# Performance work log

Measured on AMD Instinct MI355X. Metric: run time of the kernel, lower is better.

## Reference

```python
import math
import jax, jax.numpy as jnp
import numpy as np

N_ANGLES = 8
RADIUS_WIDTH = 8
OVERLAP_RATIO = 1.5
EPS = 1e-8


def _build_masks(H, W):
    # radius bin index [H,W] and normalized overlapping angular soft weights [A,H,W]
    cy, cx = H // 2, W // 2
    y, x = jnp.meshgrid(jnp.arange(H, dtype=jnp.float32), jnp.arange(W, dtype=jnp.float32), indexing='ij')
    dy, dx = y - cy, x - cx
    r = jnp.sqrt(dy ** 2 + dx ** 2)
    theta = (jnp.arctan2(dy, dx) + math.pi) % math.pi
    n_radii = int(max(cy, cx) // RADIUS_WIDTH) + 1
    radius_idx = jnp.clip(jnp.floor(r / RADIUS_WIDTH).astype(jnp.int32), 0, n_radii - 1)
    delta = math.pi / N_ANGLES
    half_width = OVERLAP_RATIO * delta / 2.0
    centers = (jnp.arange(N_ANGLES, dtype=jnp.float32) + 0.5) * delta  # [A]
    dist = jnp.abs(theta[None, :, :] - centers[:, None, None])        # [A,H,W]
    w = jnp.clip(1.0 - dist / half_width, 0.0, None) * (dist < half_width).astype(jnp.float32)
    angle_weights = w / (w.sum(axis=0, keepdims=True) + EPS)          # [A,H,W]
    return radius_idx, angle_weights, n_radii


def setup_inputs() -> dict:
    key = jax.random.key(0)
    k1, k2, k3, k4 = jax.random.split(key, 4)
    B, C, H, W = 8, 256, 128, 128
    c_mid = 16
    n_radii = (max(H // 2, W // 2) // RADIUS_WIDTH) + 1  # = 9
    x = jax.random.normal(k1, (B, C, H, W), dtype=jnp.float32)
    w_in = jax.random.normal(k2, (c_mid, C), dtype=jnp.float32) * 0.05   # 1x1 conv proj_in
    w_out = jax.random.normal(k3, (C, c_mid), dtype=jnp.float32) * 0.05  # 1x1 conv proj_out
    freq_weights = 1.0 + 0.1 * jax.random.normal(k4, (c_mid, N_ANGLES, n_radii), dtype=jnp.float32)
    return {"x": x, "w_in": w_in, "w_out": w_out, "freq_weights": freq_weights}


def reference(x, w_in, w_out, freq_weights):
    B, C, H, W = x.shape
    radius_idx, angle_weights, n_radii = _build_masks(H, W)
    # 1x1 conv in
    x_proj = jnp.einsum('bchw,mc->bmhw', x, w_in)                      # [B,c_mid,H,W]
    # FFT -> centered spectrum
    x_fft = jnp.fft.fftshift(jnp.fft.fft2(x_proj, norm='ortho'), axes=(-2, -1))
    mag = jnp.abs(x_fft) + EPS
    theta = jnp.angle(x_fft)
    # gain[c,h,w] = sum_a angle_weights[a,h,w] * freq_weights[c, a, radius_idx[h,w]]
    w_sel = freq_weights[:, :, radius_idx]                             # [c_mid,A,H,W] gather
    gain = jnp.einsum('ahw,cahw->chw', angle_weights, w_sel)           # [c_mid,H,W]
    mag_enh = mag * gain[None]                                         # [B,c_mid,H,W]
    x_fft_enh = mag_enh * jnp.exp(1j * theta)
    x_enh = jnp.fft.ifft2(jnp.fft.ifftshift(x_fft_enh, axes=(-2, -1)), norm='ortho').real
    out = x + jnp.einsum('bmhw,cm->bchw', x_enh, w_out)                # residual + 1x1 conv out
    return out
```

## Files before the change

### kernel.cpp

```cpp
#include <hip/hip_runtime.h>
#include <math.h>

#define NB   8
#define CIN  256
#define CMID 16
#define NH   128
#define NW   128
#define HWSZ 16384
#define HW4  4096
#define NANG 8
#define NRAD 9

typedef float f32x4_t __attribute__((ext_vector_type(4)));

__device__ __forceinline__ int bitrev7(int v) {
    return (int)(__brev((unsigned)v) >> 25);
}

__global__ void __launch_bounds__(256) gain_kernel(const float* __restrict__ fw,
                                                   float* __restrict__ gain) {
    int p  = blockIdx.x * 256 + threadIdx.x;
    int py = p >> 7, px = p & 127;
    int fy = bitrev7(py), fx = bitrev7(px);
    int hy = (fy + 64) & 127, hx = (fx + 64) & 127;
    float dy = (float)(hy - 64), dx = (float)(hx - 64);
    float r = sqrtf(dy * dy + dx * dx);
    int ridx = (int)floorf(r * 0.125f);
    if (ridx > NRAD - 1) ridx = NRAD - 1;
    const float PI_F = 3.14159265358979323846f;
    float theta = fmodf(atan2f(dy, dx) + PI_F, PI_F);
    const float delta = (float)(M_PI / 8.0);
    const float hwid  = (float)(1.5 * (M_PI / 8.0) / 2.0);
    float wv[NANG];
    float wsum = 0.f;
#pragma unroll
    for (int a = 0; a < NANG; ++a) {
        float c = ((float)a + 0.5f) * delta;
        float dist = fabsf(theta - c);
        float wa = fmaxf(1.0f - dist / hwid, 0.0f);
        if (!(dist < hwid)) wa = 0.0f;
        wv[a] = wa;
        wsum += wa;
    }
    float inv = 1.0f / (wsum + 1e-8f);
#pragma unroll
    for (int m = 0; m < CMID; ++m) {
        float g = 0.f;
#pragma unroll
        for (int a = 0; a < NANG; ++a)
            g += wv[a] * fw[(m * NANG + a) * NRAD + ridx];
        gain[m * HWSZ + p] = g * inv * (1.0f / 16384.0f);
    }
}

__global__ void __launch_bounds__(256, 4) proj_partial(const float* __restrict__ x,
                                                       const float* __restrict__ w_in,
                                                       float* __restrict__ partials,
                                                       int nchunk) {
    int b  = blockIdx.z;
    int ck = blockIdx.y;
    int p4 = blockIdx.x * 256 + threadIdx.x;
    int cpc = CIN / nchunk;
    int c0 = ck * cpc;
    const float4* xb = (const float4*)(x + (size_t)b * CIN * HWSZ);
    float4 acc[CMID];
#pragma unroll
    for (int m = 0; m < CMID; ++m) acc[m] = make_float4(0.f, 0.f, 0.f, 0.f);
    for (int c = c0; c < c0 + cpc; c += 4) {
        float4 v0 = xb[(size_t)(c + 0) * HW4 + p4];
        float4 v1 = xb[(size_t)(c + 1) * HW4 + p4];
        float4 v2 = xb[(size_t)(c + 2) * HW4 + p4];
        float4 v3 = xb[(size_t)(c + 3) * HW4 + p4];
#pragma unroll
        for (int m = 0; m < CMID; ++m) {
            float w0 = w_in[m * CIN + c + 0];
            float w1 = w_in[m * CIN + c + 1];
            float w2 = w_in[m * CIN + c + 2];
            float w3 = w_in[m * CIN + c + 3];
            acc[m].x = fmaf(v0.x, w0, fmaf(v1.x, w1, fmaf(v2.x, w2, fmaf(v3.x, w3, acc[m].x))));
            acc[m].y = fmaf(v0.y, w0, fmaf(v1.y, w1, fmaf(v2.y, w2, fmaf(v3.y, w3, acc[m].y))));
            acc[m].z = fmaf(v0.z, w0, fmaf(v1.z, w1, fmaf(v2.z, w2, fmaf(v3.z, w3, acc[m].z))));
            acc[m].w = fmaf(v0.w, w0, fmaf(v1.w, w1, fmaf(v2.w, w2, fmaf(v3.w, w3, acc[m].w))));
        }
    }
    float4* pb = (float4*)(partials + ((size_t)(b * nchunk + ck) * CMID) * HWSZ);
#pragma unroll
    for (int m = 0; m < CMID; ++m) pb[(size_t)m * HW4 + p4] = acc[m];
}

__global__ void __launch_bounds__(256) reduce_fft_rows(const float* __restrict__ partials,
                                                       float2* __restrict__ xf,
                                                       int nchunk) {
    __shared__ float2 lds[4 * 128];
    int img = blockIdx.y;
    int b = img >> 4, m = img & 15;
    int r0 = blockIdx.x * 4;
    int t = threadIdx.x;
#pragma unroll
    for (int ii = 0; ii < 2; ++ii) {
        int px = ii * 256 + t;
        float s = 0.f;
        for (int ck = 0; ck < nchunk; ++ck)
            s += partials[((size_t)(b * nchunk + ck) * CMID + m) * HWSZ + r0 * NW + px];
        lds[px] = make_float2(s, 0.f);
    }
    __syncthreads();
    const float PI_F = 3.14159265358979323846f;
    int j = t & 63;
    float2* row = lds + (t >> 6) * 128;
    for (int ls = 6; ls >= 0; --ls) {
        int s = 1 << ls;
        int off = j & (s - 1);
        int i0 = ((j >> ls) << (ls + 1)) + off;
        float ang = -PI_F * (float)off / (float)s;
        float sn, cs;
        __sincosf(ang, &sn, &cs);
        float2 a = row[i0];
        float2 bb = row[i0 + s];
        row[i0] = make_float2(a.x + bb.x, a.y + bb.y);
        float dx_ = a.x - bb.x, dy_ = a.y - bb.y;
        row[i0 + s] = make_float2(dx_ * cs - dy_ * sn, dx_ * sn + dy_ * cs);
        __syncthreads();
    }
#pragma unroll
    for (int ii = 0; ii < 2; ++ii) {
        int px = ii * 256 + t;
        xf[(size_t)img * HWSZ + r0 * NW + px] = lds[px];
    }
}

__global__ void __launch_bounds__(256) fft_cols_gain(float2* __restrict__ xf,
                                                     const float* __restrict__ gain) {
    __shared__ float2 buf[128 * 33];
    int img = blockIdx.y;
    int m   = img & (CMID - 1);
    int c0  = blockIdx.x * 32;
    int t   = threadIdx.x;
    float2* xi = xf + (size_t)img * HWSZ;

    for (int idx = t; idx < 128 * 32; idx += 256) {
        int r = idx >> 5, lc = idx & 31;
        buf[r * 33 + lc] = xi[r * NW + c0 + lc];
    }
    __syncthreads();
    const float PI_F = 3.14159265358979323846f;
    int lc = t & 31;
    int jb = t >> 5;
    for (int ls = 6; ls >= 0; --ls) {
        int s = 1 << ls;
        for (int j = jb; j < 64; j += 8) {
            int off = j & (s - 1);
            int i0 = ((j >> ls) << (ls + 1)) + off;
            float ang = -PI_F * (float)off / (float)s;
            float sn, cs;
            __sincosf(ang, &sn, &cs);
            float2 a = buf[i0 * 33 + lc];
            float2 bb = buf[(i0 + s) * 33 + lc];
            buf[i0 * 33 + lc] = make_float2(a.x + bb.x, a.y + bb.y);
            float dx_ = a.x - bb.x, dy_ = a.y - bb.y;
            buf[(i0 + s) * 33 + lc] = make_float2(dx_ * cs - dy_ * sn, dx_ * sn + dy_ * cs);
        }
        __syncthreads();
    }
    {
        const float* gm = gain + (size_t)m * HWSZ;
        for (int idx = t; idx < 128 * 32; idx += 256) {
            int r = idx >> 5, lcc = idx & 31;
            float g = gm[r * NW + c0 + lcc];
            buf[r * 33 + lcc].x *= g;
            buf[r * 33 + lcc].y *= g;
        }
        __syncthreads();
    }
    for (int ls = 0; ls <= 6; ++ls) {
        int s = 1 << ls;
        for (int j = jb; j < 64; j += 8) {
            int off = j & (s - 1);
            int i0 = ((j >> ls) << (ls + 1)) + off;
            float ang = PI_F * (float)off / (float)s;
            float sn, cs;
            __sincosf(ang, &sn, &cs);
            float2 a = buf[i0 * 33 + lc];
            float2 bb = buf[(i0 + s) * 33 + lc];
            float tx = bb.x * cs - bb.y * sn, ty = bb.x * sn + bb.y * cs;
            buf[i0 * 33 + lc] = make_float2(a.x + tx, a.y + ty);
            buf[(i0 + s) * 33 + lc] = make_float2(a.x - tx, a.y - ty);
        }
        __syncthreads();
    }
    for (int idx = t; idx < 128 * 32; idx += 256) {
        int r = idx >> 5, lcc = idx & 31;
        xi[r * NW + c0 + lcc] = buf[r * 33 + lcc];
    }
}

__global__ void __launch_bounds__(256) ifft_rows(const float2* __restrict__ xf,
                                                 float* __restrict__ xe) {
    __shared__ float2 lds[4 * 128];
    int img = blockIdx.y;
    int r0 = blockIdx.x * 4;
    int t = threadIdx.x;
#pragma unroll
    for (int ii = 0; ii < 2; ++ii) {
        int px = ii * 256 + t;
        lds[px] = xf[(size_t)img * HWSZ + r0 * NW + px];
    }
    __syncthreads();
    const float PI_F = 3.14159265358979323846f;
    int j = t & 63;
    float2* row = lds + (t >> 6) * 128;
    for (int ls = 0; ls <= 6; ++ls) {
        int s = 1 << ls;
        int off = j & (s - 1);
        int i0 = ((j >> ls) << (ls + 1)) + off;
        float ang = PI_F * (float)off / (float)s;
        float sn, cs;
        __sincosf(ang, &sn, &cs);
        float2 a = row[i0];
        float2 bb = row[i0 + s];
        float tx = bb.x * cs - bb.y * sn, ty = bb.x * sn + bb.y * cs;
        row[i0] = make_float2(a.x + tx, a.y + ty);
        row[i0 + s] = make_float2(a.x - tx, a.y - ty);
        __syncthreads();
    }
#pragma unroll
    for (int ii = 0; ii < 2; ++ii) {
        int px = ii * 256 + t;
        xe[(size_t)img * HWSZ + r0 * NW + px] = lds[px].x;
    }
}

__global__ void __launch_bounds__(256, 4) out_kernel(const float* __restrict__ x,
                                                     const float* __restrict__ w_out,
                                                     const float* __restrict__ xe,
                                                     float* __restrict__ out) {
    int b  = blockIdx.z;
    int ct = blockIdx.y;
    int p4 = blockIdx.x * 256 + threadIdx.x;
    const float4* xeb = (const float4*)(xe + (size_t)b * CMID * HWSZ);
    float4 e[CMID];
#pragma unroll
    for (int m = 0; m < CMID; ++m) e[m] = xeb[(size_t)m * HW4 + p4];
    const float4* xb = (const float4*)(x + (size_t)b * CIN * HWSZ);
    f32x4_t* ob = (f32x4_t*)(out + (size_t)b * CIN * HWSZ);
    int c0 = ct * 32;
    for (int c = c0; c < c0 + 32; c += 2) {
        float4 a0 = xb[(size_t)(c + 0) * HW4 + p4];
        float4 a1 = xb[(size_t)(c + 1) * HW4 + p4];
#pragma unroll
        for (int m = 0; m < CMID; ++m) {
            float w0 = w_out[(c + 0) * CMID + m];
            float w1 = w_out[(c + 1) * CMID + m];
            a0.x = fmaf(w0, e[m].x, a0.x); a0.y = fmaf(w0, e[m].y, a0.y);
            a0.z = fmaf(w0, e[m].z, a0.z); a0.w = fmaf(w0, e[m].w, a0.w);
            a1.x = fmaf(w1, e[m].x, a1.x); a1.y = fmaf(w1, e[m].y, a1.y);
            a1.z = fmaf(w1, e[m].z, a1.z); a1.w = fmaf(w1, e[m].w, a1.w);
        }
        f32x4_t s0 = { a0.x, a0.y, a0.z, a0.w };
        f32x4_t s1 = { a1.x, a1.y, a1.z, a1.w };
        __builtin_nontemporal_store(s0, ob + (size_t)(c + 0) * HW4 + p4);
        __builtin_nontemporal_store(s1, ob + (size_t)(c + 1) * HW4 + p4);
    }
}

extern "C" void kernel_launch(void* const* d_in, const int* in_sizes, int n_in,
                              void* d_out, int out_size, void* d_ws, size_t ws_size,
                              hipStream_t stream) {
    const float* x     = (const float*)d_in[0];
    const float* w_in  = (const float*)d_in[1];
    const float* w_out = (const float*)d_in[2];
    const float* fw    = (const float*)d_in[3];
    float* out = (float*)d_out;
    float* ws  = (float*)d_ws;

    int nchunk = 8;
    while (nchunk > 1) {
        size_t need = ((size_t)NB * nchunk * CMID * HWSZ +
                       (size_t)NB * CMID * HWSZ * 2 + (size_t)CMID * HWSZ) * sizeof(float);
        if (need <= ws_size) break;
        nchunk >>= 1;
    }
    float*  partials = ws;
    float2* xf   = (float2*)(ws + (size_t)NB * nchunk * CMID * HWSZ);
    float*  gain = (float*)(xf + (size_t)NB * CMID * HWSZ);
    float*  xe   = partials;

    gain_kernel<<<HWSZ / 256, 256, 0, stream>>>(fw, gain);
    proj_partial<<<dim3(HW4 / 256, nchunk, NB), 256, 0, stream>>>(x, w_in, partials, nchunk);
    reduce_fft_rows<<<dim3(NH / 4, NB * CMID), 256, 0, stream>>>(partials, xf, nchunk);
    fft_cols_gain<<<dim3(NW / 32, NB * CMID), 256, 0, stream>>>(xf, gain);
    ifft_rows<<<dim3(NH / 4, NB * CMID), 256, 0, stream>>>(xf, xe);
    out_kernel<<<dim3(HW4 / 256, CIN / 32, NB), 256, 0, stream>>>(x, w_out, xe, out);
}
```

Measured before the change: 131.1 us.

## Store intermediate partials, spectra and enhanced maps in bf16 with nontemporal loads

Converts every workspace intermediate to bf16: the proj partial sums, the complex spectrum between FFT passes (packed as two bf16 in one 32-bit word), and the enhanced spatial map read by the output kernel. It also adds nontemporal loads on the streamed x and intermediates. The goal is to roughly halve the intermediate memory traffic across all five kernels. In exchange, precision drops through the FFT pipeline, which may exceed the output tolerance.

```diff
diff --git a/kernel.cpp b/kernel.cpp
--- a/kernel.cpp
+++ b/kernel.cpp
@@ -11,7 +11,19 @@
 #define NANG 8
 #define NRAD 9
 
-typedef float f32x4_t __attribute__((ext_vector_type(4)));
+typedef float    f32x4_t __attribute__((ext_vector_type(4)));
+typedef unsigned u32x2_t __attribute__((ext_vector_type(2)));
+
+__device__ __forceinline__ unsigned short f2bf(float f) {
+    unsigned u = __float_as_uint(f);
+    u += 0x7fffu + ((u >> 16) & 1u);
+    return (unsigned short)(u >> 16);
+}
+__device__ __forceinline__ float bf_lo(unsigned u) { return __uint_as_float(u << 16); }
+__device__ __forceinline__ float bf_hi(unsigned u) { return __uint_as_float(u & 0xffff0000u); }
+__device__ __forceinline__ unsigned pack2(float a, float b) {
+    return (unsigned)f2bf(a) | ((unsigned)f2bf(b) << 16);
+}
 
 __device__ __forceinline__ int bitrev7(int v) {
     return (int)(__brev((unsigned)v) >> 25);
@@ -55,7 +67,7 @@
 
 __global__ void __launch_bounds__(256, 4) proj_partial(const float* __restrict__ x,
                                                        const float* __restrict__ w_in,
-                                                       float* __restrict__ partials,
+                                                       unsigned short* __restrict__ partials,
                                                        int nchunk) {
     int b  = blockIdx.z;
     int ck = blockIdx.y;
@@ -83,27 +95,39 @@
             acc[m].w = fmaf(v0.w, w0, fmaf(v1.w, w1, fmaf(v2.w, w2, fmaf(v3.w, w3, acc[m].w))));
         }
     }
-    float4* pb = (float4*)(partials + ((size_t)(b * nchunk + ck) * CMID) * HWSZ);
-#pragma unroll
-    for (int m = 0; m < CMID; ++m) pb[(size_t)m * HW4 + p4] = acc[m];
-}
-
-__global__ void __launch_bounds__(256) reduce_fft_rows(const float* __restrict__ partials,
-                                                       float2* __restrict__ xf,
+    ushort4* pb = (ushort4*)partials + ((size_t)(b * nchunk + ck) * CMID) * HW4;
+#pragma unroll
+    for (int m = 0; m < CMID; ++m)
+        pb[(size_t)m * HW4 + p4] = make_ushort4(f2bf(acc[m].x), f2bf(acc[m].y),
+                                                f2bf(acc[m].z), f2bf(acc[m].w));
+}
+
+__global__ void __launch_bounds__(256) reduce_fft_rows(const unsigned short* __restrict__ partials,
+                                                       unsigned* __restrict__ xf,
                                                        int nchunk) {
-    __shared__ float2 lds[4 * 128];
+    __shared__ float2 lds[512];
     int img = blockIdx.y;
     int b = img >> 4, m = img & 15;
     int r0 = blockIdx.x * 4;
     int t = threadIdx.x;
-#pragma unroll
-    for (int ii = 0; ii < 2; ++ii) {
-        int px = ii * 256 + t;
-        float s = 0.f;
-        for (int ck = 0; ck < nchunk; ++ck)
-            s += partials[((size_t)(b * nchunk + ck) * CMID + m) * HWSZ + r0 * NW + px];
-        lds[px] = make_float2(s, 0.f);
-    }
+    const unsigned* pbase = (const unsigned*)(partials +
+        ((size_t)(b * nchunk) * CMID + m) * HWSZ + (size_t)r0 * NW) + t;
+    size_t cks = (size_t)CMID * HWSZ / 2;
+    float sx = 0.f, sy = 0.f;
+    if (nchunk == 8) {
+#pragma unroll
+        for (int ck = 0; ck < 8; ++ck) {
+            unsigned u = __builtin_nontemporal_load(pbase + (size_t)ck * cks);
+            sx += bf_lo(u); sy += bf_hi(u);
+        }
+    } else {
+        for (int ck = 0; ck < nchunk; ++ck) {
+            unsigned u = __builtin_nontemporal_load(pbase + (size_t)ck * cks);
+            sx += bf_lo(u); sy += bf_hi(u);
+        }
+    }
+    lds[2 * t]     = make_float2(sx, 0.f);
+    lds[2 * t + 1] = make_float2(sy, 0.f);
     __syncthreads();
     const float PI_F = 3.14159265358979323846f;
     int j = t & 63;
@@ -122,25 +146,27 @@
         row[i0 + s] = make_float2(dx_ * cs - dy_ * sn, dx_ * sn + dy_ * cs);
         __syncthreads();
     }
+    unsigned* xo = xf + (size_t)img * HWSZ + (size_t)r0 * NW;
 #pragma unroll
     for (int ii = 0; ii < 2; ++ii) {
         int px = ii * 256 + t;
-        xf[(size_t)img * HWSZ + r0 * NW + px] = lds[px];
-    }
-}
-
-__global__ void __launch_bounds__(256) fft_cols_gain(float2* __restrict__ xf,
+        xo[px] = pack2(lds[px].x, lds[px].y);
+    }
+}
+
+__global__ void __launch_bounds__(256) fft_cols_gain(unsigned* __restrict__ xf,
                                                      const float* __restrict__ gain) {
     __shared__ float2 buf[128 * 33];
     int img = blockIdx.y;
     int m   = img & (CMID - 1);
     int c0  = blockIdx.x * 32;
     int t   = threadIdx.x;
-    float2* xi = xf + (size_t)img * HWSZ;
+    unsigned* xi = xf + (size_t)img * HWSZ;
 
     for (int idx = t; idx < 128 * 32; idx += 256) {
         int r = idx >> 5, lc = idx & 31;
-        buf[r * 33 + lc] = xi[r * NW + c0 + lc];
+        unsigned u = __builtin_nontemporal_load(&xi[r * NW + c0 + lc]);
+        buf[r * 33 + lc] = make_float2(bf_lo(u), bf_hi(u));
     }
     __syncthreads();
     const float PI_F = 3.14159265358979323846f;
@@ -190,20 +216,22 @@
     }
     for (int idx = t; idx < 128 * 32; idx += 256) {
         int r = idx >> 5, lcc = idx & 31;
-        xi[r * NW + c0 + lcc] = buf[r * 33 + lcc];
-    }
-}
-
-__global__ void __launch_bounds__(256) ifft_rows(const float2* __restrict__ xf,
-                                                 float* __restrict__ xe) {
-    __shared__ float2 lds[4 * 128];
+        xi[r * NW + c0 + lcc] = pack2(buf[r * 33 + lcc].x, buf[r * 33 + lcc].y);
+    }
+}
+
+__global__ void __launch_bounds__(256) ifft_rows(const unsigned* __restrict__ xf,
+                                                 unsigned short* __restrict__ xe) {
+    __shared__ float2 lds[512];
     int img = blockIdx.y;
     int r0 = blockIdx.x * 4;
     int t = threadIdx.x;
+    const unsigned* xi = xf + (size_t)img * HWSZ + (size_t)r0 * NW;
 #pragma unroll
     for (int ii = 0; ii < 2; ++ii) {
         int px = ii * 256 + t;
-        lds[px] = xf[(size_t)img * HWSZ + r0 * NW + px];
+        unsigned u = __builtin_nontemporal_load(&xi[px]);
+        lds[px] = make_float2(bf_lo(u), bf_hi(u));
     }
     __syncthreads();
     const float PI_F = 3.14159265358979323846f;
@@ -223,43 +251,37 @@
         row[i0 + s] = make_float2(a.x - tx, a.y - ty);
         __syncthreads();
     }
-#pragma unroll
-    for (int ii = 0; ii < 2; ++ii) {
-        int px = ii * 256 + t;
-        xe[(size_t)img * HWSZ + r0 * NW + px] = lds[px].x;
-    }
+    unsigned* xo = (unsigned*)xe + (((size_t)img * HWSZ + (size_t)r0 * NW) >> 1) + t;
+    xo[0] = pack2(lds[2 * t].x, lds[2 * t + 1].x);
 }
 
 __global__ void __launch_bounds__(256, 4) out_kernel(const float* __restrict__ x,
                                                      const float* __restrict__ w_out,
-                                                     const float* __restrict__ xe,
+                                                     const unsigned short* __restrict__ xe,
                                                      float* __restrict__ out) {
     int b  = blockIdx.z;
     int ct = blockIdx.y;
     int p4 = blockIdx.x * 256 + threadIdx.x;
-    const float4* xeb = (const float4*)(xe + (size_t)b * CMID * HWSZ);
-    float4 e[CMID];
-#pragma unroll
-    for (int m = 0; m < CMID; ++m) e[m] = xeb[(size_t)m * HW4 + p4];
-    const float4* xb = (const float4*)(x + (size_t)b * CIN * HWSZ);
+    const u32x2_t* xeb = (const u32x2_t*)(xe + (size_t)b * CMID * HWSZ);
+    f32x4_t e[CMID];
+#pragma unroll
+    for (int m = 0; m < CMID; ++m) {
+        u32x2_t u = __builtin_nontemporal_load(&xeb[(size_t)m * HW4 + p4]);
+        e[m] = (f32x4_t){ bf_lo(u.x), bf_hi(u.x), bf_lo(u.y), bf_hi(u.y) };
+    }
+    const f32x4_t* xb = (const f32x4_t*)(x + (size_t)b * CIN * HWSZ);
     f32x4_t* ob = (f32x4_t*)(out + (size_t)b * CIN * HWSZ);
     int c0 = ct * 32;
     for (int c = c0; c < c0 + 32; c += 2) {
-        float4 a0 = xb[(size_t)(c + 0) * HW4 + p4];
-        float4 a1 = xb[(size_t)(c + 1) * HW4 + p4];
+        f32x4_t a0 = __builtin_nontemporal_load(xb + (size_t)(c + 0) * HW4 + p4);
+        f32x4_t a1 = __builtin_nontemporal_load(xb + (size_t)(c + 1) * HW4 + p4);
 #pragma unroll
         for (int m = 0; m < CMID; ++m) {
-            float w0 = w_out[(c + 0) * CMID + m];
-            float w1 = w_out[(c + 1) * CMID + m];
-            a0.x = fmaf(w0, e[m].x, a0.x); a0.y = fmaf(w0, e[m].y, a0.y);
-            a0.z = fmaf(w0, e[m].z, a0.z); a0.w = fmaf(w0, e[m].w, a0.w);
-            a1.x = fmaf(w1, e[m].x, a1.x); a1.y = fmaf(w1, e[m].y, a1.y);
-            a1.z = fmaf(w1, e[m].z, a1.z); a1.w = fmaf(w1, e[m].w, a1.w);
-        }
-        f32x4_t s0 = { a0.x, a0.y, a0.z, a0.w };
-        f32x4_t s1 = { a1.x, a1.y, a1.z, a1.w };
-        __builtin_nontemporal_store(s0, ob + (size_t)(c + 0) * HW4 + p4);
-        __builtin_nontemporal_store(s1, ob + (size_t)(c + 1) * HW4 + p4);
+            a0 += w_out[(c + 0) * CMID + m] * e[m];
+            a1 += w_out[(c + 1) * CMID + m] * e[m];
+        }
+        __builtin_nontemporal_store(a0, ob + (size_t)(c + 0) * HW4 + p4);
+        __builtin_nontemporal_store(a1, ob + (size_t)(c + 1) * HW4 + p4);
     }
 }
 
@@ -271,24 +293,24 @@
     const float* w_out = (const float*)d_in[2];
     const float* fw    = (const float*)d_in[3];
     float* out = (float*)d_out;
-    float* ws  = (float*)d_ws;
 
     int nchunk = 8;
     while (nchunk > 1) {
-        size_t need = ((size_t)NB * nchunk * CMID * HWSZ +
-                       (size_t)NB * CMID * HWSZ * 2 + (size_t)CMID * HWSZ) * sizeof(float);
+        size_t need = (size_t)NB * nchunk * CMID * HWSZ * 2
+                    + (size_t)NB * CMID * HWSZ * 4
+                    + (size_t)CMID * HWSZ * 4;
         if (need <= ws_size) break;
         nchunk >>= 1;
     }
-    float*  partials = ws;
-    float2* xf   = (float2*)(ws + (size_t)NB * nchunk * CMID * HWSZ);
-    float*  gain = (float*)(xf + (size_t)NB * CMID * HWSZ);
-    float*  xe   = partials;
+    unsigned short* partials = (unsigned short*)d_ws;
+    unsigned* xfu = (unsigned*)(partials + (size_t)NB * nchunk * CMID * HWSZ);
+    float*    gain = (float*)(xfu + (size_t)NB * CMID * HWSZ);
+    unsigned short* xe = partials;
 
     gain_kernel<<<HWSZ / 256, 256, 0, stream>>>(fw, gain);
     proj_partial<<<dim3(HW4 / 256, nchunk, NB), 256, 0, stream>>>(x, w_in, partials, nchunk);
-    reduce_fft_rows<<<dim3(NH / 4, NB * CMID), 256, 0, stream>>>(partials, xf, nchunk);
-    fft_cols_gain<<<dim3(NW / 32, NB * CMID), 256, 0, stream>>>(xf, gain);
-    ifft_rows<<<dim3(NH / 4, NB * CMID), 256, 0, stream>>>(xf, xe);
+    reduce_fft_rows<<<dim3(NH / 4, NB * CMID), 256, 0, stream>>>(partials, xfu, nchunk);
+    fft_cols_gain<<<dim3(NW / 32, NB * CMID), 256, 0, stream>>>(xfu, gain);
+    ifft_rows<<<dim3(NH / 4, NB * CMID), 256, 0, stream>>>(xfu, xe);
     out_kernel<<<dim3(HW4 / 256, CIN / 32, NB), 256, 0, stream>>>(x, w_out, xe, out);
 }
```

New measurement: 126.4 us. -3.6%, faster.
